# Kernel tuning notes

Measured on AMD Instinct MI355X. Metric: run time of the kernel, lower is better.

The kernel has to match this reference:

```python
import jax, jax.numpy as jnp
from jax import lax
import numpy as np

D_MODEL = 96; D_STATE = 16; SSM_RATIO = 2.0; D_CONV = 3; K = 4
D_INNER = int(SSM_RATIO * D_MODEL)      # 192
DT_RANK = -(-D_MODEL // 16)             # ceil(96/16) = 6
B_SZ = 4; H = 32; W = 32

# ---- zig-zag (snake) index helpers (static numpy) ----
def _snake_h(Hh, Ww):
    idx = np.tile(np.arange(Ww), (Hh, 1)); idx[1::2] = idx[1::2, ::-1]; return idx  # (H,W)

def _snake_v(Hh, Ww):
    idx = np.tile(np.arange(Hh)[:, None], (1, Ww)); idx[:, 1::2] = idx[::-1, 1::2]; return idx  # (H,W)

def _h_scan(x, d):
    Hh, Ww = x.shape[-2:]
    if d == 'left':
        x = jnp.flip(x, (-1, -2))
    return x[:, :, np.arange(Hh)[:, None], _snake_h(Hh, Ww)]

def _v_scan(x, d):
    Bb, Cc, Hh, Ww = x.shape
    if d == 'up':
        x = jnp.flip(x, (-1, -2))
    t = x[:, :, _snake_v(Hh, Ww), np.arange(Ww)[None, :]]  # gather along H per column
    return jnp.swapaxes(t, -1, -2).reshape(Bb, Cc, Hh, Ww)

def _h_merge(x, d):
    Hh, Ww = x.shape[-2:]
    t = x[:, :, np.arange(Hh)[:, None], _snake_h(Hh, Ww)]
    if d == 'left':
        t = jnp.flip(t, (-1, -2))
    return t

def _v_merge(x, d):
    Hh, Ww = x.shape[-2:]
    t2 = jnp.swapaxes(x, -1, -2)  # (B,C,W,H); requires H==W like the torch source
    t = t2[:, :, _snake_v(Hh, Ww), np.arange(Ww)[None, :]]
    if d == 'up':
        t = jnp.flip(t, (-1, -2))
    return t

def cross_scan(x):
    return jnp.stack([_v_scan(x, 'down'), _v_scan(x, 'up'), _h_scan(x, 'right'), _h_scan(x, 'left')], axis=1)

def cross_merge(ys):
    return (_v_merge(ys[:, 0], 'down') + _v_merge(ys[:, 1], 'up')
            + _h_merge(ys[:, 2], 'right') + _h_merge(ys[:, 3], 'left'))

def selective_scan(u, delta, A, Bs, Cs, Dp, delta_bias):
    # u,delta:(B,K,D,L)  A:(K,D,N)  Bs,Cs:(B,K,N,L)  Dp,delta_bias:(K,D)
    delta = jax.nn.softplus(delta + delta_bias[None, :, :, None])
    dA = jnp.exp(jnp.einsum('bkdl,kdn->lbkdn', delta, A))
    dBu = jnp.einsum('bkdl,bkdl,bknl->lbkdn', delta, u, Bs)
    Ct = jnp.moveaxis(Cs, -1, 0)  # (L,B,K,N)
    def step(h, inp):
        dA_t, dBu_t, c_t = inp
        h = dA_t * h + dBu_t
        return h, jnp.einsum('bkdn,bkn->bkd', h, c_t)
    h0 = jnp.zeros(dA.shape[1:], u.dtype)
    _, ys = lax.scan(step, h0, (dA, dBu, Ct))
    return jnp.moveaxis(ys, 0, -1) + Dp[None, :, :, None] * u  # (B,K,D,L)

def setup_inputs() -> dict:
    key = jax.random.key(0)
    ks = jax.random.split(key, 8)
    x = jax.random.normal(ks[0], (B_SZ, D_MODEL, H, W), jnp.float32)
    in_proj_w = jax.random.normal(ks[1], (2 * D_INNER, D_MODEL), jnp.float32) * (D_MODEL ** -0.5)
    conv_w = jax.random.normal(ks[2], (D_INNER, 1, D_CONV, D_CONV), jnp.float32) * 0.2  # depthwise
    conv_b = jnp.zeros((D_INNER,), jnp.float32)
    x_proj_w = jax.random.normal(ks[3], (K, DT_RANK + 2 * D_STATE, D_INNER), jnp.float32) * (D_INNER ** -0.5)
    s = DT_RANK ** -0.5
    dt_w = jax.random.uniform(ks[4], (K, D_INNER, DT_RANK), jnp.float32, -s, s)
    dt = jax.random.uniform(ks[5], (K, D_INNER), jnp.float32, 0.001, 0.1)
    dt_b = jnp.log(jnp.expm1(dt))  # inverse softplus, as in dt_init
    A_logs = jnp.tile(jnp.log(jnp.arange(1, D_STATE + 1, dtype=jnp.float32)), (K * D_INNER, 1))
    Ds = jnp.ones((K * D_INNER,), jnp.float32)
    gn_gamma = jnp.ones((D_INNER,), jnp.float32)
    gn_beta = jnp.zeros((D_INNER,), jnp.float32)
    out_proj_w = jax.random.normal(ks[6], (D_MODEL, D_INNER), jnp.float32) * (D_INNER ** -0.5)
    return {'x': x, 'in_proj_w': in_proj_w, 'conv_w': conv_w, 'conv_b': conv_b,
            'x_proj_w': x_proj_w, 'dt_w': dt_w, 'dt_b': dt_b, 'A_logs': A_logs, 'Ds': Ds,
            'gn_gamma': gn_gamma, 'gn_beta': gn_beta, 'out_proj_w': out_proj_w}

def reference(x, in_proj_w, conv_w, conv_b, x_proj_w, dt_w, dt_b, A_logs, Ds, gn_gamma, gn_beta, out_proj_w):
    Bb, _, Hh, Ww = x.shape; L = Hh * Ww
    xz = jnp.einsum('bchw,oc->bohw', x, in_proj_w)          # in_proj (1x1 conv, no bias)
    xx, z = jnp.split(xz, 2, axis=1)
    z = jax.nn.silu(z)
    xx = lax.conv_general_dilated(xx, conv_w, (1, 1), 'SAME', feature_group_count=D_INNER,
                                  dimension_numbers=('NCHW', 'OIHW', 'NCHW')) + conv_b[None, :, None, None]
    xx = jax.nn.silu(xx)
    xs = cross_scan(xx).reshape(Bb, K, D_INNER, L)          # 4-direction zig-zag scan
    x_dbl = jnp.einsum('bkdl,kcd->bkcl', xs, x_proj_w)
    dts = jnp.einsum('bkrl,kdr->bkdl', x_dbl[:, :, :DT_RANK], dt_w)
    Bs = x_dbl[:, :, DT_RANK:DT_RANK + D_STATE]
    Cs = x_dbl[:, :, DT_RANK + D_STATE:]
    A = -jnp.exp(A_logs).reshape(K, D_INNER, D_STATE)
    y = selective_scan(xs, dts, A, Bs, Cs, Ds.reshape(K, D_INNER), dt_b)
    y = cross_merge(y.reshape(Bb, K, D_INNER, Hh, Ww))       # (B,D,H,W)
    # out_norm: GroupNorm(1, d_inner) == layernorm over (C,H,W) per sample
    mu = jnp.mean(y, axis=(1, 2, 3), keepdims=True)
    var = jnp.var(y, axis=(1, 2, 3), keepdims=True)
    y = (y - mu) * lax.rsqrt(var + 1e-6)
    y = y * gn_gamma[None, :, None, None] + gn_beta[None, :, None, None]
    y = y * z
    return jnp.einsum('bchw,oc->bohw', y, out_proj_w)
```

## Files before the change

### kernel.cpp

```cpp
#include <hip/hip_runtime.h>
#include <math.h>

#define Bsz 4
#define DM 96
#define DI 192
#define NS 16
#define RK 6
#define KK 4
#define HH 32
#define WW 32
#define LL 1024
#define NC 32
#define CS 32

__device__ __forceinline__ float silu_f(float x) { return x / (1.f + __expf(-x)); }

__device__ __forceinline__ int hw_of_l(int k, int l) {
    int a = l >> 5, r = l & 31;
    int m = (a & 1) ? 31 - r : r;
    int h, w;
    if (k < 2) { w = a; h = m; }
    else       { h = a; w = m; }
    if (k & 1) { h = 31 - h; w = 31 - w; }
    return h * 32 + w;
}

__global__ void in_proj_k(const float* __restrict__ x, const float* __restrict__ w,
                          float* __restrict__ xx, float* __restrict__ zs,
                          float* __restrict__ stats) {
    int bi = blockIdx.x;
    int t = threadIdx.x;
    if (bi == 0 && t < 2 * Bsz) stats[t] = 0.f;
    int lb = bi & 3;
    int og = (bi >> 2) % 48;
    int b = bi / 192;
    int l = lb * 256 + t;
    const float* xb = x + (size_t)b * DM * LL + l;
    float acc[8];
#pragma unroll
    for (int g = 0; g < 8; g++) acc[g] = 0.f;
    for (int c = 0; c < DM; c++) {
        float xv = xb[(size_t)c * LL];
#pragma unroll
        for (int g = 0; g < 8; g++)
            acc[g] = fmaf(xv, w[(size_t)(og * 8 + g) * DM + c], acc[g]);
    }
#pragma unroll
    for (int g = 0; g < 8; g++) {
        int o = og * 8 + g;
        if (o < DI) xx[((size_t)b * DI + o) * LL + l] = acc[g];
        else        zs[((size_t)b * DI + (o - DI)) * LL + l] = silu_f(acc[g]);
    }
}

__global__ void convT_k(const float* __restrict__ xx, const float* __restrict__ cw,
                        const float* __restrict__ cb, float* __restrict__ xxT) {
    __shared__ float tile[32][65];
    int bi = blockIdx.x;
    int h0 = bi % 32;
    int dt = (bi / 32) % 3;
    int b = bi / 96;
    int d0 = dt * 64;
    int t = threadIdx.x;
    int wi = t & 31, dg = t >> 5;

#pragma unroll
    for (int pass = 0; pass < 8; pass++) {
        int di = pass * 8 + dg;
        int d = d0 + di;
        const float* xp = xx + ((size_t)b * DI + d) * LL;
        const float* wp = cw + d * 9;
        float acc = cb[d];
#pragma unroll
        for (int kh = 0; kh < 3; kh++) {
            int hh = h0 + kh - 1;
            if (hh < 0 || hh >= HH) continue;
#pragma unroll
            for (int kw = 0; kw < 3; kw++) {
                int ww2 = wi + kw - 1;
                if (ww2 < 0 || ww2 >= WW) continue;
                acc = fmaf(xp[hh * WW + ww2], wp[kh * 3 + kw], acc);
            }
        }
        tile[wi][di] = silu_f(acc);
    }
    __syncthreads();

    int di = t & 63, w4 = t >> 6;
#pragma unroll
    for (int rep = 0; rep < 8; rep++) {
        int w2 = rep * 4 + w4;
        xxT[((size_t)b * LL + h0 * 32 + w2) * DI + d0 + di] = tile[w2][di];
    }
}

__global__ void __launch_bounds__(512)
xdbl_k(const float* __restrict__ xxT, const float* __restrict__ xpw,
       float* __restrict__ xdbl) {
    __shared__ float tile[64 * 193];
    int blk = blockIdx.x;
    int bk = blk >> 4, lt = blk & 15;
    int k = bk & 3, b = bk >> 2;
    int t = threadIdx.x;

    const float* xb = xxT + (size_t)b * LL * DI;
#pragma unroll
    for (int i = 0; i < 6; i++) {
        int j4 = t + i * 512;
        int lr = j4 / 48;
        int d4 = j4 % 48;
        int hw = hw_of_l(k, lt * 64 + lr);
        float4 v = ((const float4*)(xb + (size_t)hw * DI))[d4];
        float* dst = &tile[lr * 193 + d4 * 4];
        dst[0] = v.x; dst[1] = v.y; dst[2] = v.z; dst[3] = v.w;
    }
    __syncthreads();

    int ll = t & 63;
    int cg = t >> 6;
    int c0 = cg * 5;
    int wlim = (c0 + 5 <= 38) ? 5 : (38 - c0);
    const float* wk = xpw + (size_t)k * 38 * DI;

    float acc[5];
#pragma unroll
    for (int j = 0; j < 5; j++) acc[j] = 0.f;
    const float* xrow = &tile[ll * 193];
#pragma unroll 4
    for (int d = 0; d < DI; d++) {
        float xv = xrow[d];
#pragma unroll
        for (int j = 0; j < 5; j++) {
            int cc = c0 + j; cc = (cc > 37) ? 37 : cc;
            acc[j] = fmaf(xv, wk[(size_t)cc * DI + d], acc[j]);
        }
    }
    float* orow = xdbl + ((size_t)bk * LL + lt * 64 + ll) * 38;
#pragma unroll
    for (int j = 0; j < 5; j++)
        if (j < wlim) orow[c0 + j] = acc[j];
}

__global__ void scan_p1(const float* __restrict__ xxT, const float* __restrict__ xdbl,
                        const float* __restrict__ dtw_g, const float* __restrict__ dtb_g,
                        const float* __restrict__ Alog,
                        float* __restrict__ Pst, float* __restrict__ Hloc) {
    int blk = blockIdx.x;
    int bk = blk / NC, c = blk % NC;
    int k = bk & 3, b = bk >> 2;
    int d = threadIdx.x;
    int kd = k * DI + d;

    float A[NS];
#pragma unroll
    for (int n = 0; n < NS; n++) A[n] = -__expf(Alog[(size_t)kd * NS + n]);
    float dtw[RK];
#pragma unroll
    for (int r = 0; r < RK; r++) dtw[r] = dtw_g[(size_t)kd * RK + r];
    float dtb = dtb_g[kd];

    float h[NS], P[NS];
#pragma unroll
    for (int n = 0; n < NS; n++) { h[n] = 0.f; P[n] = 1.f; }

    const float* xdbase = xdbl + ((size_t)bk * LL + c * CS) * 38;
    const float* xb = xxT + (size_t)b * LL * DI;

    for (int s = 0; s < CS; s++) {
        const float* xd = xdbase + s * 38;
        int hw = hw_of_l(k, c * CS + s);
        float u = xb[(size_t)hw * DI + d];
        float dt = dtb;
#pragma unroll
        for (int r = 0; r < RK; r++) dt = fmaf(xd[r], dtw[r], dt);
        dt = (dt > 20.f) ? dt : __logf(1.f + __expf(dt));
        float du = dt * u;
#pragma unroll
        for (int n = 0; n < NS; n++) {
            float a = __expf(dt * A[n]);
            h[n] = fmaf(a, h[n], du * xd[6 + n]);
            P[n] *= a;
        }
    }
    size_t base = ((size_t)blk * DI + d) * NS;
#pragma unroll
    for (int n = 0; n < NS; n++) { Pst[base + n] = P[n]; Hloc[base + n] = h[n]; }
}

__global__ void scan_mid(const float* __restrict__ Pst, float* __restrict__ Hloc) {
    int gid = blockIdx.x * 256 + threadIdx.x;
    int bk = gid / 1536;
    int j = gid % 1536;
    const float2* Pp = (const float2*)(Pst + (size_t)bk * NC * (DI * NS)) + j;
    float2* Hp = (float2*)(Hloc + (size_t)bk * NC * (DI * NS)) + j;
    const int S = (DI * NS) / 2;

    float2 h = make_float2(0.f, 0.f);
    float2 P[4], L[4];
#pragma unroll
    for (int q = 0; q < 4; q++) { P[q] = Pp[(size_t)q * S]; L[q] = Hp[(size_t)q * S]; }
    for (int c = 0; c < NC; c += 4) {
        float2 Pn[4], Ln[4];
        if (c + 4 < NC) {
#pragma unroll
            for (int q = 0; q < 4; q++) {
                Pn[q] = Pp[(size_t)(c + 4 + q) * S];
                Ln[q] = Hp[(size_t)(c + 4 + q) * S];
            }
        }
#pragma unroll
        for (int q = 0; q < 4; q++) {
            Hp[(size_t)(c + q) * S] = h;
            h.x = fmaf(P[q].x, h.x, L[q].x);
            h.y = fmaf(P[q].y, h.y, L[q].y);
        }
#pragma unroll
        for (int q = 0; q < 4; q++) { P[q] = Pn[q]; L[q] = Ln[q]; }
    }
}

__global__ void scan_p3(const float* __restrict__ xxT, const float* __restrict__ xdbl,
                        const float* __restrict__ dtw_g, const float* __restrict__ dtb_g,
                        const float* __restrict__ Alog, const float* __restrict__ Ds,
                        const float* __restrict__ Hin, float* __restrict__ ysm) {
    int blk = blockIdx.x;
    int bk = blk / NC, c = blk % NC;
    int k = bk & 3, b = bk >> 2;
    int d = threadIdx.x;
    int kd = k * DI + d;

    float A[NS];
#pragma unroll
    for (int n = 0; n < NS; n++) A[n] = -__expf(Alog[(size_t)kd * NS + n]);
    float dtw[RK];
#pragma unroll
    for (int r = 0; r < RK; r++) dtw[r] = dtw_g[(size_t)kd * RK + r];
    float dtb = dtb_g[kd];
    float Dp = Ds[kd];

    float h[NS];
    size_t hbase = ((size_t)blk * DI + d) * NS;
#pragma unroll
    for (int n = 0; n < NS; n++) h[n] = Hin[hbase + n];

    const float* xdbase = xdbl + ((size_t)bk * LL + c * CS) * 38;
    const float* xb = xxT + (size_t)b * LL * DI;
    float* yk = ysm + (size_t)bk * LL * DI;

    for (int s = 0; s < CS; s++) {
        const float* xd = xdbase + s * 38;
        int hw = hw_of_l(k, c * CS + s);
        float u = xb[(size_t)hw * DI + d];
        float dt = dtb;
#pragma unroll
        for (int r = 0; r < RK; r++) dt = fmaf(xd[r], dtw[r], dt);
        dt = (dt > 20.f) ? dt : __logf(1.f + __expf(dt));
        float du = dt * u;
        float y = 0.f;
#pragma unroll
        for (int n = 0; n < NS; n++) {
            float a = __expf(dt * A[n]);
            h[n] = fmaf(a, h[n], du * xd[6 + n]);
            y = fmaf(h[n], xd[22 + n], y);
        }
        yk[(size_t)hw * DI + d] = fmaf(Dp, u, y);
    }
}

#define MT 16
__global__ void merge_k(const float* __restrict__ ysm, float* __restrict__ ym,
                        float* __restrict__ stats) {
    __shared__ float tile[MT][DI + 1];
    __shared__ float sh1[3], sh2[3];
    int b = blockIdx.y;
    int hw0 = blockIdx.x * MT;
    int d = threadIdx.x;
    const float* yb = ysm + (size_t)b * KK * LL * DI;

    float s1 = 0.f, s2 = 0.f;
#pragma unroll
    for (int hwi = 0; hwi < MT; hwi++) {
        int hw = hw0 + hwi;
        float v = yb[((size_t)0 * LL + hw) * DI + d]
                + yb[((size_t)1 * LL + hw) * DI + d]
                + yb[((size_t)2 * LL + hw) * DI + d]
                + yb[((size_t)3 * LL + hw) * DI + d];
        tile[hwi][d] = v;
        s1 += v; s2 = fmaf(v, v, s2);
    }
#pragma unroll
    for (int off = 32; off > 0; off >>= 1) {
        s1 += __shfl_down(s1, off);
        s2 += __shfl_down(s2, off);
    }
    int lane = threadIdx.x & 63, wid = threadIdx.x >> 6;
    if (lane == 0) { sh1[wid] = s1; sh2[wid] = s2; }
    __syncthreads();
    if (threadIdx.x == 0) {
        atomicAdd(&stats[b * 2],     sh1[0] + sh1[1] + sh1[2]);
        atomicAdd(&stats[b * 2 + 1], sh2[0] + sh2[1] + sh2[2]);
    }
#pragma unroll
    for (int rep = 0; rep < MT; rep++) {
        int j = rep * DI + threadIdx.x;
        int d2 = j >> 4;
        int hwi = j & (MT - 1);
        ym[((size_t)b * DI + d2) * LL + hw0 + hwi] = tile[hwi][d2];
    }
}

__global__ void yz_k(const float* __restrict__ ym, const float* __restrict__ zs,
                     const float* __restrict__ g, const float* __restrict__ be,
                     const float* __restrict__ stats, float* __restrict__ yz) {
    int idx = blockIdx.x * 256 + threadIdx.x;
    int c = (idx >> 10) % DI;
    int b = idx / (LL * DI);
    const float Ninv = 1.f / (float)(DI * LL);
    float mu = stats[b * 2] * Ninv;
    float var = stats[b * 2 + 1] * Ninv - mu * mu;
    float rstd = rsqrtf(var + 1e-6f);
    float v = (ym[idx] - mu) * rstd * g[c] + be[c];
    yz[idx] = v * zs[idx];
}

__global__ void out_k(const float* __restrict__ yz, const float* __restrict__ wo,
                      float* __restrict__ out) {
    int bi = blockIdx.x;
    int t = threadIdx.x;
    int lb = bi & 3;
    int og = (bi >> 2) % 24;
    int b = bi / 96;
    int l = lb * 256 + t;
    const float* yb = yz + (size_t)b * DI * LL + l;
    float acc[4];
#pragma unroll
    for (int g = 0; g < 4; g++) acc[g] = 0.f;
    for (int c = 0; c < DI; c++) {
        float yv = yb[(size_t)c * LL];
#pragma unroll
        for (int g = 0; g < 4; g++)
            acc[g] = fmaf(yv, wo[(size_t)(og * 4 + g) * DI + c], acc[g]);
    }
#pragma unroll
    for (int g = 0; g < 4; g++)
        out[((size_t)b * DM + og * 4 + g) * LL + l] = acc[g];
}

extern "C" void kernel_launch(void* const* d_in, const int* in_sizes, int n_in,
                              void* d_out, int out_size, void* d_ws, size_t ws_size,
                              hipStream_t stream) {
    const float* x    = (const float*)d_in[0];
    const float* ipw  = (const float*)d_in[1];
    const float* cw   = (const float*)d_in[2];
    const float* cb   = (const float*)d_in[3];
    const float* xpw  = (const float*)d_in[4];
    const float* dtw  = (const float*)d_in[5];
    const float* dtb  = (const float*)d_in[6];
    const float* Alog = (const float*)d_in[7];
    const float* Ds   = (const float*)d_in[8];
    const float* gng  = (const float*)d_in[9];
    const float* gnb  = (const float*)d_in[10];
    const float* opw  = (const float*)d_in[11];
    float* out = (float*)d_out;

    float* ws = (float*)d_ws;
    const size_t o_xx   = 0;
    const size_t o_zs   = o_xx   + (size_t)Bsz * DI * LL;
    const size_t o_xxT  = o_zs   + (size_t)Bsz * DI * LL;
    const size_t o_xdbl = o_xxT  + (size_t)Bsz * LL * DI;
    const size_t o_P    = o_xdbl + (size_t)Bsz * KK * LL * 38;
    const size_t o_H    = o_P    + (size_t)Bsz * KK * NC * DI * NS;
    const size_t o_ysm  = o_H    + (size_t)Bsz * KK * NC * DI * NS;
    const size_t o_st   = o_ysm  + (size_t)Bsz * KK * LL * DI;

    float* xx    = ws + o_xx;
    float* zs    = ws + o_zs;
    float* xxT   = ws + o_xxT;
    float* xdbl  = ws + o_xdbl;
    float* Pst   = ws + o_P;
    float* Hst   = ws + o_H;
    float* ysm   = ws + o_ysm;
    float* stats = ws + o_st;
    float* ym = xx;
    float* yz = Pst;

    hipLaunchKernelGGL(in_proj_k, dim3(768), dim3(256), 0, stream, x, ipw, xx, zs, stats);
    hipLaunchKernelGGL(convT_k, dim3(384), dim3(256), 0, stream, xx, cw, cb, xxT);
    hipLaunchKernelGGL(xdbl_k, dim3(256), dim3(512), 0, stream, xxT, xpw, xdbl);
    hipLaunchKernelGGL(scan_p1, dim3(Bsz * KK * NC), dim3(192), 0, stream,
                       xxT, xdbl, dtw, dtb, Alog, Pst, Hst);
    hipLaunchKernelGGL(scan_mid, dim3(96), dim3(256), 0, stream, Pst, Hst);
    hipLaunchKernelGGL(scan_p3, dim3(Bsz * KK * NC), dim3(192), 0, stream,
                       xxT, xdbl, dtw, dtb, Alog, Ds, Hst, ysm);
    hipLaunchKernelGGL(merge_k, dim3(LL / MT, Bsz), dim3(192), 0, stream, ysm, ym, stats);
    hipLaunchKernelGGL(yz_k, dim3(3072), dim3(256), 0, stream, ym, zs, gng, gnb, stats, yz);
    hipLaunchKernelGGL(out_k, dim3(384), dim3(256), 0, stream, yz, opw, out);
}
```

Measured before the change: 211.8 us.

## Refine scan chunking, stage xdbl in LDS, fuse norm into out-proj, retune grids

Doubles the number of scan chunks (NC 32 to 64, CS 32 to 16) so more blocks run the selective scan. Both scan phases now copy each chunk's x_dbl rows into shared memory before the recurrence. The in_proj, convT and merge kernels get smaller per-block tiles and larger grids. The group-norm and z-gating step is fused into the output projection, which removes the yz buffer write and read. The trade-offs are more work in the inter-chunk prefix pass, extra P/H state storage, and the norm being recomputed once per output-channel group.

```diff
diff --git a/kernel.cpp b/kernel.cpp
--- a/kernel.cpp
+++ b/kernel.cpp
@@ -10,8 +10,8 @@
 #define HH 32
 #define WW 32
 #define LL 1024
-#define NC 32
-#define CS 32
+#define NC 64
+#define CS 16
 
 __device__ __forceinline__ float silu_f(float x) { return x / (1.f + __expf(-x)); }
 
@@ -32,22 +32,22 @@
     int t = threadIdx.x;
     if (bi == 0 && t < 2 * Bsz) stats[t] = 0.f;
     int lb = bi & 3;
-    int og = (bi >> 2) % 48;
-    int b = bi / 192;
+    int og = (bi >> 2) % 96;
+    int b = bi / 384;
     int l = lb * 256 + t;
     const float* xb = x + (size_t)b * DM * LL + l;
-    float acc[8];
-#pragma unroll
-    for (int g = 0; g < 8; g++) acc[g] = 0.f;
+    float acc[4];
+#pragma unroll
+    for (int g = 0; g < 4; g++) acc[g] = 0.f;
     for (int c = 0; c < DM; c++) {
         float xv = xb[(size_t)c * LL];
 #pragma unroll
-        for (int g = 0; g < 8; g++)
-            acc[g] = fmaf(xv, w[(size_t)(og * 8 + g) * DM + c], acc[g]);
-    }
-#pragma unroll
-    for (int g = 0; g < 8; g++) {
-        int o = og * 8 + g;
+        for (int g = 0; g < 4; g++)
+            acc[g] = fmaf(xv, w[(size_t)(og * 4 + g) * DM + c], acc[g]);
+    }
+#pragma unroll
+    for (int g = 0; g < 4; g++) {
+        int o = og * 4 + g;
         if (o < DI) xx[((size_t)b * DI + o) * LL + l] = acc[g];
         else        zs[((size_t)b * DI + (o - DI)) * LL + l] = silu_f(acc[g]);
     }
@@ -55,17 +55,17 @@
 
 __global__ void convT_k(const float* __restrict__ xx, const float* __restrict__ cw,
                         const float* __restrict__ cb, float* __restrict__ xxT) {
-    __shared__ float tile[32][65];
+    __shared__ float tile[32][33];
     int bi = blockIdx.x;
     int h0 = bi % 32;
-    int dt = (bi / 32) % 3;
-    int b = bi / 96;
-    int d0 = dt * 64;
+    int dt = (bi / 32) % 6;
+    int b = bi / 192;
+    int d0 = dt * 32;
     int t = threadIdx.x;
     int wi = t & 31, dg = t >> 5;
 
 #pragma unroll
-    for (int pass = 0; pass < 8; pass++) {
+    for (int pass = 0; pass < 4; pass++) {
         int di = pass * 8 + dg;
         int d = d0 + di;
         const float* xp = xx + ((size_t)b * DI + d) * LL;
@@ -86,10 +86,10 @@
     }
     __syncthreads();
 
-    int di = t & 63, w4 = t >> 6;
-#pragma unroll
-    for (int rep = 0; rep < 8; rep++) {
-        int w2 = rep * 4 + w4;
+    int di = t & 31, w8 = t >> 5;
+#pragma unroll
+    for (int rep = 0; rep < 4; rep++) {
+        int w2 = rep * 8 + w8;
         xxT[((size_t)b * LL + h0 * 32 + w2) * DI + d0 + di] = tile[w2][di];
     }
 }
@@ -145,10 +145,17 @@
                         const float* __restrict__ dtw_g, const float* __restrict__ dtb_g,
                         const float* __restrict__ Alog,
                         float* __restrict__ Pst, float* __restrict__ Hloc) {
+    __shared__ float xd_tile[CS * 38];
     int blk = blockIdx.x;
     int bk = blk / NC, c = blk % NC;
     int k = bk & 3, b = bk >> 2;
-    int d = threadIdx.x;
+    int t = threadIdx.x;
+
+    const float* xdsrc = xdbl + ((size_t)bk * LL + c * CS) * 38;
+    for (int i = t; i < CS * 38; i += 192) xd_tile[i] = xdsrc[i];
+    __syncthreads();
+
+    int d = t;
     int kd = k * DI + d;
 
     float A[NS];
@@ -163,11 +170,10 @@
 #pragma unroll
     for (int n = 0; n < NS; n++) { h[n] = 0.f; P[n] = 1.f; }
 
-    const float* xdbase = xdbl + ((size_t)bk * LL + c * CS) * 38;
     const float* xb = xxT + (size_t)b * LL * DI;
 
     for (int s = 0; s < CS; s++) {
-        const float* xd = xdbase + s * 38;
+        const float* xd = &xd_tile[s * 38];
         int hw = hw_of_l(k, c * CS + s);
         float u = xb[(size_t)hw * DI + d];
         float dt = dtb;
@@ -223,10 +229,17 @@
                         const float* __restrict__ dtw_g, const float* __restrict__ dtb_g,
                         const float* __restrict__ Alog, const float* __restrict__ Ds,
                         const float* __restrict__ Hin, float* __restrict__ ysm) {
+    __shared__ float xd_tile[CS * 38];
     int blk = blockIdx.x;
     int bk = blk / NC, c = blk % NC;
     int k = bk & 3, b = bk >> 2;
-    int d = threadIdx.x;
+    int t = threadIdx.x;
+
+    const float* xdsrc = xdbl + ((size_t)bk * LL + c * CS) * 38;
+    for (int i = t; i < CS * 38; i += 192) xd_tile[i] = xdsrc[i];
+    __syncthreads();
+
+    int d = t;
     int kd = k * DI + d;
 
     float A[NS];
@@ -243,12 +256,11 @@
 #pragma unroll
     for (int n = 0; n < NS; n++) h[n] = Hin[hbase + n];
 
-    const float* xdbase = xdbl + ((size_t)bk * LL + c * CS) * 38;
     const float* xb = xxT + (size_t)b * LL * DI;
     float* yk = ysm + (size_t)bk * LL * DI;
 
     for (int s = 0; s < CS; s++) {
-        const float* xd = xdbase + s * 38;
+        const float* xd = &xd_tile[s * 38];
         int hw = hw_of_l(k, c * CS + s);
         float u = xb[(size_t)hw * DI + d];
         float dt = dtb;
@@ -267,7 +279,7 @@
     }
 }
 
-#define MT 16
+#define MT 4
 __global__ void merge_k(const float* __restrict__ ysm, float* __restrict__ ym,
                         float* __restrict__ stats) {
     __shared__ float tile[MT][DI + 1];
@@ -303,47 +315,43 @@
 #pragma unroll
     for (int rep = 0; rep < MT; rep++) {
         int j = rep * DI + threadIdx.x;
-        int d2 = j >> 4;
+        int d2 = j >> 2;
         int hwi = j & (MT - 1);
         ym[((size_t)b * DI + d2) * LL + hw0 + hwi] = tile[hwi][d2];
     }
 }
 
-__global__ void yz_k(const float* __restrict__ ym, const float* __restrict__ zs,
-                     const float* __restrict__ g, const float* __restrict__ be,
-                     const float* __restrict__ stats, float* __restrict__ yz) {
-    int idx = blockIdx.x * 256 + threadIdx.x;
-    int c = (idx >> 10) % DI;
-    int b = idx / (LL * DI);
+__global__ void outz_k(const float* __restrict__ ym, const float* __restrict__ zs,
+                       const float* __restrict__ g, const float* __restrict__ be,
+                       const float* __restrict__ stats, const float* __restrict__ wo,
+                       float* __restrict__ out) {
+    int bi = blockIdx.x;
+    int t = threadIdx.x;
+    int lb = bi & 3;
+    int og = (bi >> 2) % 32;
+    int b = bi / 128;
+    int l = lb * 256 + t;
+
     const float Ninv = 1.f / (float)(DI * LL);
     float mu = stats[b * 2] * Ninv;
     float var = stats[b * 2 + 1] * Ninv - mu * mu;
     float rstd = rsqrtf(var + 1e-6f);
-    float v = (ym[idx] - mu) * rstd * g[c] + be[c];
-    yz[idx] = v * zs[idx];
-}
-
-__global__ void out_k(const float* __restrict__ yz, const float* __restrict__ wo,
-                      float* __restrict__ out) {
-    int bi = blockIdx.x;
-    int t = threadIdx.x;
-    int lb = bi & 3;
-    int og = (bi >> 2) % 24;
-    int b = bi / 96;
-    int l = lb * 256 + t;
-    const float* yb = yz + (size_t)b * DI * LL + l;
-    float acc[4];
-#pragma unroll
-    for (int g = 0; g < 4; g++) acc[g] = 0.f;
+
+    const float* yb = ym + (size_t)b * DI * LL + l;
+    const float* zb = zs + (size_t)b * DI * LL + l;
+    float acc[3];
+#pragma unroll
+    for (int gg = 0; gg < 3; gg++) acc[gg] = 0.f;
     for (int c = 0; c < DI; c++) {
-        float yv = yb[(size_t)c * LL];
-#pragma unroll
-        for (int g = 0; g < 4; g++)
-            acc[g] = fmaf(yv, wo[(size_t)(og * 4 + g) * DI + c], acc[g]);
-    }
-#pragma unroll
-    for (int g = 0; g < 4; g++)
-        out[((size_t)b * DM + og * 4 + g) * LL + l] = acc[g];
+        float v = (yb[(size_t)c * LL] - mu) * rstd * g[c] + be[c];
+        float yv = v * zb[(size_t)c * LL];
+#pragma unroll
+        for (int gg = 0; gg < 3; gg++)
+            acc[gg] = fmaf(yv, wo[(size_t)(og * 3 + gg) * DI + c], acc[gg]);
+    }
+#pragma unroll
+    for (int gg = 0; gg < 3; gg++)
+        out[((size_t)b * DM + og * 3 + gg) * LL + l] = acc[gg];
 }
 
 extern "C" void kernel_launch(void* const* d_in, const int* in_sizes, int n_in,
@@ -382,10 +390,9 @@
     float* ysm   = ws + o_ysm;
     float* stats = ws + o_st;
     float* ym = xx;
-    float* yz = Pst;
-
-    hipLaunchKernelGGL(in_proj_k, dim3(768), dim3(256), 0, stream, x, ipw, xx, zs, stats);
-    hipLaunchKernelGGL(convT_k, dim3(384), dim3(256), 0, stream, xx, cw, cb, xxT);
+
+    hipLaunchKernelGGL(in_proj_k, dim3(1536), dim3(256), 0, stream, x, ipw, xx, zs, stats);
+    hipLaunchKernelGGL(convT_k, dim3(768), dim3(256), 0, stream, xx, cw, cb, xxT);
     hipLaunchKernelGGL(xdbl_k, dim3(256), dim3(512), 0, stream, xxT, xpw, xdbl);
     hipLaunchKernelGGL(scan_p1, dim3(Bsz * KK * NC), dim3(192), 0, stream,
                        xxT, xdbl, dtw, dtb, Alog, Pst, Hst);
@@ -393,6 +400,5 @@
     hipLaunchKernelGGL(scan_p3, dim3(Bsz * KK * NC), dim3(192), 0, stream,
                        xxT, xdbl, dtw, dtb, Alog, Ds, Hst, ysm);
     hipLaunchKernelGGL(merge_k, dim3(LL / MT, Bsz), dim3(192), 0, stream, ysm, ym, stats);
-    hipLaunchKernelGGL(yz_k, dim3(3072), dim3(256), 0, stream, ym, zs, gng, gnb, stats, yz);
-    hipLaunchKernelGGL(out_k, dim3(384), dim3(256), 0, stream, yz, opw, out);
-}
+    hipLaunchKernelGGL(outz_k, dim3(512), dim3(256), 0, stream, ym, zs, gng, gnb, stats, opw, out);
+}
```

Result: slower. 219.5 us (+3.7%).
